# Optimization experiments

Measured on AMD Instinct MI355X. Metric: run time of the kernel, lower is better.

Reference implementation:

```python
import jax, jax.numpy as jnp
import numpy as np

N, H, V = 8192, 1024, 32000
IGNORE_INDEX = -100
LABEL_SMOOTHING = 0.0
LOGIT_SCALE = 1.0


def setup_inputs() -> dict:
    key = jax.random.key(0)
    k1, k2, k3 = jax.random.split(key, 3)
    x = jax.random.normal(k1, (N, H), dtype=jnp.float32)
    weight = jax.random.normal(k2, (V, H), dtype=jnp.float32) * 0.02
    bias = jnp.zeros((V,), dtype=jnp.float32)
    target = jax.random.randint(k3, (N,), 0, V, dtype=jnp.int64)
    return {"x": x, "weight": weight, "bias": bias, "target": target}


def reference(x, weight, bias, target):
    # logits: [N, V]; fused kernel never materializes this fully, but math is identical
    logits = (x @ weight.T + bias) * LOGIT_SCALE
    lse = jax.nn.logsumexp(logits.astype(jnp.float32), axis=-1)  # [N]
    valid = target != IGNORE_INDEX
    safe_t = jnp.where(valid, target, 0)
    tgt_logit = jnp.take_along_axis(logits, safe_t[:, None], axis=-1)[:, 0]
    loss_i = lse - tgt_logit
    if LABEL_SMOOTHING > 0:
        eps = LABEL_SMOOTHING / V
        z = (-eps * logits).sum(-1)
        loss_i = loss_i * (1.0 - LABEL_SMOOTHING) + (z + LABEL_SMOOTHING * lse)
    loss_i = jnp.where(valid, loss_i, 0.0)
    total = jnp.maximum(valid.sum(), 1)
    # reduction == 'mean': each per-token loss divided by total, then summed
    return loss_i.sum() / total
```

## Files before the change

kernel.cpp:

```cpp
#include <hip/hip_runtime.h>
#include <math.h>

typedef int    intx8    __attribute__((ext_vector_type(8)));
typedef float  floatx16 __attribute__((ext_vector_type(16)));

#define N_ROWS 8192
#define H_DIM  1024
#define V_DIM  32000
#define V_PAD  32768
#define IGNORE_INDEX (-100)

#define S_SPLITS 16
#define TILES_PER_SPLIT 16
#define BM 256
#define BN 128
#define BK 64

#define LOG2E 1.4426950408889634f
#define LN2   0.6931471805599453f

__device__ __forceinline__ void conv_one(const float* __restrict__ in,
                                         unsigned char* __restrict__ out,
                                         int r, int u, int Rstride, float scale) {
  const float4* src = (const float4*)(in + (size_t)r * H_DIM + u * 16);
  uint4 res;
#pragma unroll
  for (int j = 0; j < 4; ++j) {
    const float4 v = src[j];
    int p = __builtin_amdgcn_cvt_pk_fp8_f32(v.x * scale, v.y * scale, 0, false);
    p = __builtin_amdgcn_cvt_pk_fp8_f32(v.z * scale, v.w * scale, p, true);
    ((int*)&res)[j] = p;
  }
  *(uint4*)(out + ((size_t)u * Rstride + r) * 16) = res;
}

__global__ __launch_bounds__(256) void prep_all(const float* __restrict__ x,
                                                const float* __restrict__ wgt,
                                                const float* __restrict__ bias,
                                                const int* __restrict__ target,
                                                unsigned char* __restrict__ xs8,
                                                unsigned char* __restrict__ ws8,
                                                float* __restrict__ biasp,
                                                float* __restrict__ tgt_logit) {
  const int bid = blockIdx.x;
  const int tid = threadIdx.x;
  if (bid < 8000) {
    conv_one(wgt, ws8, (bid % 125) * 256 + tid, bid / 125, V_PAD, 1.0f);
  } else if (bid < 10048) {
    const int b = bid - 8000;
    conv_one(x, xs8, (b % 32) * 256 + tid, b / 32, N_ROWS, LOG2E);
  } else if (bid < 10176) {
    const int i = (bid - 10048) * 256 + tid;
    biasp[i] = (i < V_DIM) ? bias[i] * LOG2E : -1e30f;
  } else {
    const int r = (bid - 10176) * 4 + (tid >> 6);
    const int lane = tid & 63;
    const int t = target[r];
    const int tt = (t == IGNORE_INDEX) ? 0 : t;
    const float4* xr = (const float4*)(x + (size_t)r * H_DIM);
    const float4* wr = (const float4*)(wgt + (size_t)tt * H_DIM);
    float acc = 0.f;
#pragma unroll
    for (int i = 0; i < 4; ++i) {
      const float4 a = xr[lane + i * 64];
      const float4 b = wr[lane + i * 64];
      acc += a.x * b.x + a.y * b.y + a.z * b.z + a.w * b.w;
    }
#pragma unroll
    for (int off = 32; off >= 1; off >>= 1) acc += __shfl_xor(acc, off, 64);
    if (lane == 0) tgt_logit[r] = acc + bias[tt];
  }
}

__global__ __launch_bounds__(256, 2) void flce_main(const unsigned char* __restrict__ xs,
                                                    const unsigned char* __restrict__ wsb,
                                                    const float* __restrict__ biasp,
                                                    float* __restrict__ partials) {
  __shared__ __align__(16) unsigned char smA[2][4 * 256 * 16];
  __shared__ __align__(16) unsigned char smB[2][4 * 128 * 16];

  const int tid  = threadIdx.x;
  const int lane = tid & 63;
  const int w    = tid >> 6;
  const int l31  = lane & 31;
  const int half = lane >> 5;
  const int wr   = w * 64;
  const int row0 = blockIdx.x * BM;
  const int sidx = blockIdx.y;

  float l_state[32];
#pragma unroll
  for (int i = 0; i < 32; ++i) l_state[i] = 0.f;

  floatx16 acc[2][4];
#pragma unroll
  for (int mb = 0; mb < 2; ++mb)
#pragma unroll
    for (int nb = 0; nb < 4; ++nb)
#pragma unroll
      for (int i = 0; i < 16; ++i) acc[mb][nb][i] = 0.f;

  auto issue_dma = [&](int f, int p) {
    const int ct = f >> 4;
    const int k  = f & 15;
    const int n0 = (sidx * TILES_PER_SPLIT + ct) * BN;
    const int ub = k * 4;
#pragma unroll
    for (int j = 0; j < 4; ++j) {
      const int c = j * 4 + w;
      const int u = c >> 2;
      const int rb = c & 3;
      __builtin_amdgcn_global_load_lds(
          (const __attribute__((address_space(1))) void*)(xs + ((size_t)(ub + u) * N_ROWS + row0 + rb * 64 + lane) * 16),
          (__attribute__((address_space(3))) void*)(smA[p] + ((u * 256 + rb * 64 + lane) * 16)),
          16, 0, 0);
    }
#pragma unroll
    for (int j = 0; j < 2; ++j) {
      const int c = j * 4 + w;
      const int u = c >> 1;
      const int rb = c & 1;
      __builtin_amdgcn_global_load_lds(
          (const __attribute__((address_space(1))) void*)(wsb + ((size_t)(ub + u) * V_PAD + n0 + rb * 64 + lane) * 16),
          (__attribute__((address_space(3))) void*)(smB[p] + ((u * 128 + rb * 64 + lane) * 16)),
          16, 0, 0);
    }
  };

  issue_dma(0, 0);
  __syncthreads();

  float bnb[4];
  const int ua = half * 2;

#pragma unroll 1
  for (int f = 0; f < TILES_PER_SPLIT * 16; ++f) {
    const int p = f & 1;
    if (f + 1 < TILES_PER_SPLIT * 16) issue_dma(f + 1, p ^ 1);

    if ((f & 15) == 0) {
      const int n0 = (sidx * TILES_PER_SPLIT + (f >> 4)) * BN;
#pragma unroll
      for (int nb = 0; nb < 4; ++nb) bnb[nb] = biasp[n0 + nb * 32 + l31];
    }

    union { intx8 v; uint4 q[2]; } a[2], b[4];
#pragma unroll
    for (int mb = 0; mb < 2; ++mb) {
      a[mb].q[0] = *(const uint4*)(smA[p] + ((ua * 256 + wr + mb * 32 + l31) * 16));
      a[mb].q[1] = *(const uint4*)(smA[p] + (((ua + 1) * 256 + wr + mb * 32 + l31) * 16));
    }
#pragma unroll
    for (int nb = 0; nb < 4; ++nb) {
      b[nb].q[0] = *(const uint4*)(smB[p] + ((ua * 128 + nb * 32 + l31) * 16));
      b[nb].q[1] = *(const uint4*)(smB[p] + (((ua + 1) * 128 + nb * 32 + l31) * 16));
    }
#pragma unroll
    for (int mb = 0; mb < 2; ++mb)
#pragma unroll
      for (int nb = 0; nb < 4; ++nb)
        acc[mb][nb] = __builtin_amdgcn_mfma_scale_f32_32x32x64_f8f6f4(
            a[mb].v, b[nb].v, acc[mb][nb],
            0, 0,
            0, 0x7F7F7F7F,
            0, 0x7F7F7F7F);

    if ((f & 15) == 15) {
#pragma unroll
      for (int mb = 0; mb < 2; ++mb)
#pragma unroll
        for (int r = 0; r < 16; ++r) {
          l_state[mb * 16 + r] += __builtin_amdgcn_exp2f(acc[mb][0][r] + bnb[0])
                                + __builtin_amdgcn_exp2f(acc[mb][1][r] + bnb[1])
                                + __builtin_amdgcn_exp2f(acc[mb][2][r] + bnb[2])
                                + __builtin_amdgcn_exp2f(acc[mb][3][r] + bnb[3]);
        }
#pragma unroll
      for (int mb = 0; mb < 2; ++mb)
#pragma unroll
        for (int nb = 0; nb < 4; ++nb)
#pragma unroll
          for (int i = 0; i < 16; ++i) acc[mb][nb][i] = 0.f;
    }
    __syncthreads();
  }

#pragma unroll
  for (int s = 0; s < 32; ++s) {
    float v = l_state[s];
#pragma unroll
    for (int off = 1; off < 32; off <<= 1) v += __shfl_xor(v, off, 64);
    l_state[s] = v;
  }

  if (l31 == 0) {
#pragma unroll
    for (int s = 0; s < 32; ++s) {
      const int mb = s >> 4, r = s & 15;
      const int row = wr + mb * 32 + 4 * half + (r & 3) + 8 * (r >> 2);
      partials[(size_t)(row0 + row) * S_SPLITS + sidx] = l_state[s];
    }
  }
}

__global__ __launch_bounds__(256) void loss_rows(const float* __restrict__ partials,
                                                 const float* __restrict__ tgt_logit,
                                                 const int* __restrict__ target,
                                                 float* __restrict__ bsums) {
  const int r = blockIdx.x * 256 + threadIdx.x;
  float l = 0.f;
#pragma unroll
  for (int s = 0; s < S_SPLITS; ++s) l += partials[(size_t)r * S_SPLITS + s];
  const float lse = LN2 * __log2f(l);
  const bool valid = (target[r] != IGNORE_INDEX);
  float loss = valid ? (lse - tgt_logit[r]) : 0.f;
  float cnt  = valid ? 1.f : 0.f;
  const int lane = threadIdx.x & 63;
  const int w = threadIdx.x >> 6;
#pragma unroll
  for (int off = 32; off >= 1; off >>= 1) {
    loss += __shfl_xor(loss, off, 64);
    cnt  += __shfl_xor(cnt, off, 64);
  }
  __shared__ float sl[4], sc[4];
  if (lane == 0) { sl[w] = loss; sc[w] = cnt; }
  __syncthreads();
  if (threadIdx.x == 0) {
    float S = 0.f, C = 0.f;
    for (int i = 0; i < 4; ++i) { S += sl[i]; C += sc[i]; }
    bsums[blockIdx.x] = S;
    bsums[32 + blockIdx.x] = C;
  }
}

__global__ void finalize(const float* __restrict__ bsums, float* __restrict__ out) {
  const int t = threadIdx.x;
  float s = (t < 32) ? bsums[t] : 0.f;
  float c = (t < 32) ? bsums[32 + t] : 0.f;
#pragma unroll
  for (int off = 32; off >= 1; off >>= 1) {
    s += __shfl_xor(s, off, 64);
    c += __shfl_xor(c, off, 64);
  }
  if (t == 0) out[0] = s / fmaxf(c, 1.f);
}

extern "C" void kernel_launch(void* const* d_in, const int* in_sizes, int n_in,
                              void* d_out, int out_size, void* d_ws, size_t ws_size,
                              hipStream_t stream) {
  const float* x    = (const float*)d_in[0];
  const float* wgt  = (const float*)d_in[1];
  const float* bias = (const float*)d_in[2];
  const int*   tgt  = (const int*)d_in[3];
  float* out = (float*)d_out;

  char* ws = (char*)d_ws;
  const size_t XS8 = (size_t)N_ROWS * H_DIM;
  const size_t WS8 = (size_t)V_PAD * H_DIM;
  const size_t BP  = (size_t)V_PAD * 4;
  const size_t PB  = (size_t)N_ROWS * S_SPLITS * 4;
  unsigned char* xs8 = (unsigned char*)ws;
  unsigned char* ws8 = (unsigned char*)(ws + XS8);
  float* biasp    = (float*)(ws + XS8 + WS8);
  float* partials = (float*)(ws + XS8 + WS8 + BP);
  float* tgt_lg   = (float*)(ws + XS8 + WS8 + BP + PB);
  float* bsums    = (float*)(ws + XS8 + WS8 + BP + PB + (size_t)N_ROWS * 4);

  prep_all<<<12224, 256, 0, stream>>>(x, wgt, bias, tgt, xs8, ws8, biasp, tgt_lg);
  flce_main<<<dim3(N_ROWS / BM, S_SPLITS), 256, 0, stream>>>(xs8, ws8, biasp, partials);
  loss_rows<<<N_ROWS / 256, 256, 0, stream>>>(partials, tgt_lg, tgt, bsums);
  finalize<<<1, 64, 0, stream>>>(bsums, out);
}
```

Before: 498.3 us.

## Fold bias into GEMM as extra K unit and triple-buffer weight tiles

The bias is now appended as a 17th K-step. The x side gets a column holding 1.0 in fp8 and the weight side gets the fp8-quantized bias times log2e, with a large negative value for padded vocab rows. This removes the per-tile bias loads and adds from the epilogue. The main loop is also rebuilt with a ring of three B buffers and manual waitcnt/barrier placement so loads for the next step can overlap compute. The costs are one extra MFMA step per tile (17 instead of 16) and lower bias precision, since it is rounded to fp8.

```diff
diff --git a/kernel.cpp b/kernel.cpp
--- a/kernel.cpp
+++ b/kernel.cpp
@@ -6,6 +6,7 @@
 
 #define N_ROWS 8192
 #define H_DIM  1024
+#define UNITS  68
 #define V_DIM  32000
 #define V_PAD  32768
 #define IGNORE_INDEX (-100)
@@ -14,7 +15,8 @@
 #define TILES_PER_SPLIT 16
 #define BM 256
 #define BN 128
-#define BK 64
+#define KSTEPS 17
+#define NSTEPS (TILES_PER_SPLIT * KSTEPS)
 
 #define LOG2E 1.4426950408889634f
 #define LN2   0.6931471805599453f
@@ -40,7 +42,6 @@
                                                 const int* __restrict__ target,
                                                 unsigned char* __restrict__ xs8,
                                                 unsigned char* __restrict__ ws8,
-                                                float* __restrict__ biasp,
                                                 float* __restrict__ tgt_logit) {
   const int bid = blockIdx.x;
   const int tid = threadIdx.x;
@@ -50,10 +51,30 @@
     const int b = bid - 8000;
     conv_one(x, xs8, (b % 32) * 256 + tid, b / 32, N_ROWS, LOG2E);
   } else if (bid < 10176) {
-    const int i = (bid - 10048) * 256 + tid;
-    biasp[i] = (i < V_DIM) ? bias[i] * LOG2E : -1e30f;
+    const int r = (bid - 10048) * 256 + tid;
+    uint4 z = {0, 0, 0, 0};
+    unsigned char b0;
+    if (r < V_DIM) {
+      const int p = __builtin_amdgcn_cvt_pk_fp8_f32(bias[r] * LOG2E, 0.f, 0, false);
+      b0 = (unsigned char)(p & 0xFF);
+    } else {
+      b0 = 0xFE;
+    }
+    ((unsigned char*)&z)[0] = b0;
+    *(uint4*)(ws8 + ((size_t)64 * V_PAD + r) * 16) = z;
+  } else if (bid < 10208) {
+    const int r = (bid - 10176) * 256 + tid;
+    uint4 z = {0, 0, 0, 0};
+    ((unsigned char*)&z)[0] = 0x38;
+    *(uint4*)(xs8 + ((size_t)64 * N_ROWS + r) * 16) = z;
+  } else if (bid < 10304) {
+    const int b = bid - 10208;
+    const int u = 65 + b / 32;
+    const int r = (b % 32) * 256 + tid;
+    const uint4 z = {0, 0, 0, 0};
+    *(uint4*)(xs8 + ((size_t)u * N_ROWS + r) * 16) = z;
   } else {
-    const int r = (bid - 10176) * 4 + (tid >> 6);
+    const int r = (bid - 10304) * 4 + (tid >> 6);
     const int lane = tid & 63;
     const int t = target[r];
     const int tt = (t == IGNORE_INDEX) ? 0 : t;
@@ -74,10 +95,9 @@
 
 __global__ __launch_bounds__(256, 2) void flce_main(const unsigned char* __restrict__ xs,
                                                     const unsigned char* __restrict__ wsb,
-                                                    const float* __restrict__ biasp,
                                                     float* __restrict__ partials) {
   __shared__ __align__(16) unsigned char smA[2][4 * 256 * 16];
-  __shared__ __align__(16) unsigned char smB[2][4 * 128 * 16];
+  __shared__ __align__(16) unsigned char smB[3][4 * 128 * 16];
 
   const int tid  = threadIdx.x;
   const int lane = tid & 63;
@@ -86,7 +106,7 @@
   const int half = lane >> 5;
   const int wr   = w * 64;
   const int row0 = blockIdx.x * BM;
-  const int sidx = blockIdx.y;
+  const int n0base = blockIdx.y * TILES_PER_SPLIT * BN;
 
   float l_state[32];
 #pragma unroll
@@ -100,10 +120,7 @@
 #pragma unroll
       for (int i = 0; i < 16; ++i) acc[mb][nb][i] = 0.f;
 
-  auto issue_dma = [&](int f, int p) {
-    const int ct = f >> 4;
-    const int k  = f & 15;
-    const int n0 = (sidx * TILES_PER_SPLIT + ct) * BN;
+  auto issue_A = [&](int k, int p) {
     const int ub = k * 4;
 #pragma unroll
     for (int j = 0; j < 4; ++j) {
@@ -115,6 +132,9 @@
           (__attribute__((address_space(3))) void*)(smA[p] + ((u * 256 + rb * 64 + lane) * 16)),
           16, 0, 0);
     }
+  };
+  auto issue_B = [&](int k, int n0, int p) {
+    const int ub = k * 4;
 #pragma unroll
     for (int j = 0; j < 2; ++j) {
       const int c = j * 4 + w;
@@ -127,34 +147,49 @@
     }
   };
 
-  issue_dma(0, 0);
-  __syncthreads();
-
-  float bnb[4];
+  issue_B(0, n0base, 0);
+  issue_A(0, 0);
+  issue_B(1, n0base, 1);
+
+  int kk = 0;
+  int kA = 1;
+  int kB = 2, n0B = n0base;
+  int pB = 0, pBi = 2;
+  int sidx_out = 0;
+
   const int ua = half * 2;
 
 #pragma unroll 1
-  for (int f = 0; f < TILES_PER_SPLIT * 16; ++f) {
-    const int p = f & 1;
-    if (f + 1 < TILES_PER_SPLIT * 16) issue_dma(f + 1, p ^ 1);
-
-    if ((f & 15) == 0) {
-      const int n0 = (sidx * TILES_PER_SPLIT + (f >> 4)) * BN;
-#pragma unroll
-      for (int nb = 0; nb < 4; ++nb) bnb[nb] = biasp[n0 + nb * 32 + l31];
+  for (int f = 0; f < NSTEPS; ++f) {
+    if (f == NSTEPS - 1)
+      asm volatile("s_waitcnt vmcnt(0) lgkmcnt(0)\ns_barrier" ::: "memory");
+    else
+      asm volatile("s_waitcnt vmcnt(2) lgkmcnt(0)\ns_barrier" ::: "memory");
+
+    const int pA = f & 1;
+    if (f + 1 < NSTEPS) {
+      issue_A(kA, pA ^ 1);
+      kA = (kA == KSTEPS - 1) ? 0 : kA + 1;
+    }
+    if (f + 2 < NSTEPS) {
+      issue_B(kB, n0B, pBi);
+      if (++kB == KSTEPS) { kB = 0; n0B += BN; }
+      if (++pBi == 3) pBi = 0;
     }
 
     union { intx8 v; uint4 q[2]; } a[2], b[4];
 #pragma unroll
     for (int mb = 0; mb < 2; ++mb) {
-      a[mb].q[0] = *(const uint4*)(smA[p] + ((ua * 256 + wr + mb * 32 + l31) * 16));
-      a[mb].q[1] = *(const uint4*)(smA[p] + (((ua + 1) * 256 + wr + mb * 32 + l31) * 16));
+      a[mb].q[0] = *(const uint4*)(smA[pA] + ((ua * 256 + wr + mb * 32 + l31) * 16));
+      a[mb].q[1] = *(const uint4*)(smA[pA] + (((ua + 1) * 256 + wr + mb * 32 + l31) * 16));
     }
 #pragma unroll
     for (int nb = 0; nb < 4; ++nb) {
-      b[nb].q[0] = *(const uint4*)(smB[p] + ((ua * 128 + nb * 32 + l31) * 16));
-      b[nb].q[1] = *(const uint4*)(smB[p] + (((ua + 1) * 128 + nb * 32 + l31) * 16));
-    }
+      b[nb].q[0] = *(const uint4*)(smB[pB] + ((ua * 128 + nb * 32 + l31) * 16));
+      b[nb].q[1] = *(const uint4*)(smB[pB] + (((ua + 1) * 128 + nb * 32 + l31) * 16));
+    }
+    if (++pB == 3) pB = 0;
+
 #pragma unroll
     for (int mb = 0; mb < 2; ++mb)
 #pragma unroll
@@ -165,15 +200,15 @@
             0, 0x7F7F7F7F,
             0, 0x7F7F7F7F);
 
-    if ((f & 15) == 15) {
+    if (kk == KSTEPS - 1) {
 #pragma unroll
       for (int mb = 0; mb < 2; ++mb)
 #pragma unroll
         for (int r = 0; r < 16; ++r) {
-          l_state[mb * 16 + r] += __builtin_amdgcn_exp2f(acc[mb][0][r] + bnb[0])
-                                + __builtin_amdgcn_exp2f(acc[mb][1][r] + bnb[1])
-                                + __builtin_amdgcn_exp2f(acc[mb][2][r] + bnb[2])
-                                + __builtin_amdgcn_exp2f(acc[mb][3][r] + bnb[3]);
+          l_state[mb * 16 + r] += __builtin_amdgcn_exp2f(acc[mb][0][r])
+                                + __builtin_amdgcn_exp2f(acc[mb][1][r])
+                                + __builtin_amdgcn_exp2f(acc[mb][2][r])
+                                + __builtin_amdgcn_exp2f(acc[mb][3][r]);
         }
 #pragma unroll
       for (int mb = 0; mb < 2; ++mb)
@@ -181,8 +216,11 @@
         for (int nb = 0; nb < 4; ++nb)
 #pragma unroll
           for (int i = 0; i < 16; ++i) acc[mb][nb][i] = 0.f;
-    }
-    __syncthreads();
+      kk = 0;
+      ++sidx_out;
+    } else {
+      ++kk;
+    }
   }
 
 #pragma unroll
@@ -198,7 +236,7 @@
     for (int s = 0; s < 32; ++s) {
       const int mb = s >> 4, r = s & 15;
       const int row = wr + mb * 32 + 4 * half + (r & 3) + 8 * (r >> 2);
-      partials[(size_t)(row0 + row) * S_SPLITS + sidx] = l_state[s];
+      partials[(size_t)(row0 + row) * S_SPLITS + blockIdx.y] = l_state[s];
     }
   }
 }
@@ -255,19 +293,17 @@
   float* out = (float*)d_out;
 
   char* ws = (char*)d_ws;
-  const size_t XS8 = (size_t)N_ROWS * H_DIM;
-  const size_t WS8 = (size_t)V_PAD * H_DIM;
-  const size_t BP  = (size_t)V_PAD * 4;
+  const size_t XS8 = (size_t)UNITS * N_ROWS * 16;
+  const size_t WS8 = (size_t)UNITS * V_PAD * 16;
   const size_t PB  = (size_t)N_ROWS * S_SPLITS * 4;
   unsigned char* xs8 = (unsigned char*)ws;
   unsigned char* ws8 = (unsigned char*)(ws + XS8);
-  float* biasp    = (float*)(ws + XS8 + WS8);
-  float* partials = (float*)(ws + XS8 + WS8 + BP);
-  float* tgt_lg   = (float*)(ws + XS8 + WS8 + BP + PB);
-  float* bsums    = (float*)(ws + XS8 + WS8 + BP + PB + (size_t)N_ROWS * 4);
-
-  prep_all<<<12224, 256, 0, stream>>>(x, wgt, bias, tgt, xs8, ws8, biasp, tgt_lg);
-  flce_main<<<dim3(N_ROWS / BM, S_SPLITS), 256, 0, stream>>>(xs8, ws8, biasp, partials);
+  float* partials = (float*)(ws + XS8 + WS8);
+  float* tgt_lg   = (float*)(ws + XS8 + WS8 + PB);
+  float* bsums    = (float*)(ws + XS8 + WS8 + PB + (size_t)N_ROWS * 4);
+
+  prep_all<<<12352, 256, 0, stream>>>(x, wgt, bias, tgt, xs8, ws8, tgt_lg);
+  flce_main<<<dim3(N_ROWS / BM, S_SPLITS), 256, 0, stream>>>(xs8, ws8, partials);
   loss_rows<<<N_ROWS / 256, 256, 0, stream>>>(partials, tgt_lg, tgt, bsums);
   finalize<<<1, 64, 0, stream>>>(bsums, out);
 }
```

Measured after the change: 531.6 us. 6.7% more time.
